# Kernel optimization log

Measured on AMD Instinct MI355X. Metric: run time of the kernel, lower is better.

## Reference

```python
import jax, jax.numpy as jnp
import numpy as np

TEMPERATURE = 0.1
BATCH_SIZE = 64
EPS = 1e-8  # torch.nn.CosineSimilarity eps
NEG_INF = -1e30

B, C, D = 64, 16, 512  # batch, children per sample, feature dim


def setup_inputs() -> dict:
    key = jax.random.key(0)
    k1, k2, k3, k4 = jax.random.split(key, 4)
    children_is = jax.random.normal(k1, (B, C, D), dtype=jnp.float32)
    children_js = jax.random.normal(k2, (B, C, D), dtype=jnp.float32)
    partnet_ids = jnp.arange(B, dtype=jnp.int64 if jax.config.jax_enable_x64 else jnp.int32)
    neg_idx_j = jax.random.randint(k3, (B, B, C), 0, C)  # negatives drawn from children_js
    neg_idx_k = jax.random.randint(k4, (B, B, C), 0, C)  # negatives drawn from children_is
    return {
        "children_is": children_is,
        "children_js": children_js,
        "partnet_ids": partnet_ids,
        "neg_idx_j": neg_idx_j,
        "neg_idx_k": neg_idx_k,
    }


def _safe_norm(x, axis=-1):
    return jnp.maximum(jnp.sqrt(jnp.sum(x * x, axis=axis)), EPS)


def _ntxent(ci, cj, pids, nj, nk):
    b = ci.shape[0]
    fi = ci.reshape(b, -1)  # [B, L] flattened anchors
    fj = cj.reshape(b, -1)  # [B, L] flattened positives
    norm_i = _safe_norm(fi)

    # positive: cos(flat(children_i), flat(children_j[i])) / T
    pos = jnp.sum(fi * fj, axis=-1) / (norm_i * _safe_norm(fj))  # [B]

    src = jnp.arange(b)[None, :, None]  # broadcast source-sample index
    # gathered negatives: g*[i, j] = children_*[j, neg_idx[i, j]] flattened -> [B, B, L]
    gj = cj[src, nj].reshape(b, b, -1)
    gk = ci[src, nk].reshape(b, b, -1)

    sim_j = jnp.einsum('il,ijl->ij', fi, gj) / (norm_i[:, None] * _safe_norm(gj))
    sim_k = jnp.einsum('il,ijl->ij', fi, gk) / (norm_i[:, None] * _safe_norm(gk))

    # negative pair valid iff j != i and partnet ids differ
    eye = jnp.arange(b)
    mask = (eye[None, :] != eye[:, None]) & (pids[None, :] != pids[:, None])  # [B, B]

    logits = jnp.concatenate(
        [pos[:, None],
         jnp.where(mask, sim_j, NEG_INF),
         jnp.where(mask, sim_k, NEG_INF)], axis=1) / TEMPERATURE  # [B, 1+2B]

    # CrossEntropy with label 0, reduction='sum' over the batch of anchors
    loss = jnp.sum(-logits[:, 0] + jax.scipy.special.logsumexp(logits, axis=1))
    return loss / (2.0 * BATCH_SIZE)


def reference(children_is, children_js, partnet_ids, neg_idx_j, neg_idx_k):
    return _ntxent(children_is, children_js, partnet_ids, neg_idx_j, neg_idx_k)
```

## Files before the change

### kernel.cpp

```cpp
#include <hip/hip_runtime.h>
#include <math.h>

#define BB 64
#define CC 16
#define DD 512
#define LL 8192
#define EPSV 1e-8f
#define INVT 10.0f
#define NEGINF_T (-1e31f)

#define WS_N2I 0
#define WS_N2J 1024
#define WS_DJ  2048
#define WS_DK  6144
#define WS_POS 10240

__device__ __forceinline__ float dot4(float4 a, float4 b) {
    return a.x * b.x + a.y * b.y + a.z * b.z + a.w * b.w;
}

__device__ __forceinline__ float wave_reduce(float v) {
    #pragma unroll
    for (int off = 32; off; off >>= 1) v += __shfl_down(v, off);
    return v;
}

__global__ __launch_bounds__(256) void ntx_prep(const float* __restrict__ ci,
                                                const float* __restrict__ cj,
                                                float* __restrict__ ws,
                                                float* __restrict__ out) {
    const int b = blockIdx.x, tid = threadIdx.x;
    __shared__ float red[4];
    if (b < 512) {
        const int row  = b * 4 + (tid >> 6);
        const int lane = tid & 63;
        const int r    = row & 1023;
        const float4* src = (const float4*)(row < 1024 ? ci : cj);
        float4 v1 = src[r * 128 + lane];
        float4 v2 = src[r * 128 + 64 + lane];
        float acc = dot4(v1, v1) + dot4(v2, v2);
        acc = wave_reduce(acc);
        if (lane == 0) ws[(row < 1024 ? WS_N2I : WS_N2J) + r] = acc;
    } else {
        const int i = b - 512;
        if (b == 512 && tid == 0) out[0] = 0.f;
        const float4* fi = (const float4*)(ci + i * LL);
        const float4* fj = (const float4*)(cj + i * LL);
        float acc = 0.f;
        #pragma unroll
        for (int it = 0; it < 8; ++it) acc += dot4(fi[tid + 256 * it], fj[tid + 256 * it]);
        acc = wave_reduce(acc);
        if ((tid & 63) == 0) red[tid >> 6] = acc;
        __syncthreads();
        if (tid == 0) ws[WS_POS + i] = red[0] + red[1] + red[2] + red[3];
    }
}

__global__ __launch_bounds__(256) void ntx_sim(const float* __restrict__ ci,
                                               const float* __restrict__ cj,
                                               const int* __restrict__ nj,
                                               const int* __restrict__ nk,
                                               float* __restrict__ ws) {
    const int jt  = blockIdx.x;
    const int i   = blockIdx.y;
    const int tid = threadIdx.x;

    __shared__ int   sidx[2][4][16];
    __shared__ float red[4][2][4];

    if (tid < 64)        ((int*)sidx)[tid] = nj[i * 1024 + jt * 64 + tid];
    else if (tid < 128)  ((int*)sidx)[tid] = nk[i * 1024 + jt * 64 + (tid - 64)];

    const float4* fi4 = (const float4*)(ci + i * LL);
    float4 fiv[8];
    #pragma unroll
    for (int it = 0; it < 8; ++it) fiv[it] = fi4[tid + 256 * it];

    __syncthreads();

    const int d4   = tid & 127;
    const int half = tid >> 7;
    const float4* cj4 = (const float4*)cj;
    const float4* ci4 = (const float4*)ci;

    #pragma unroll
    for (int jj = 0; jj < 4; ++jj) {
        const int j = jt * 4 + jj;
        const float4* bj = cj4 + j * CC * 128;
        const float4* bk = ci4 + j * CC * 128;
        float aj = 0.f, ak = 0.f;
        #pragma unroll
        for (int it = 0; it < 8; ++it) {
            const int c = half + 2 * it;
            float4 vj = bj[sidx[0][jj][c] * 128 + d4];
            float4 vk = bk[sidx[1][jj][c] * 128 + d4];
            aj += dot4(fiv[it], vj);
            ak += dot4(fiv[it], vk);
        }
        aj = wave_reduce(aj);
        ak = wave_reduce(ak);
        if ((tid & 63) == 0) { red[jj][0][tid >> 6] = aj; red[jj][1][tid >> 6] = ak; }
    }
    __syncthreads();
    if (tid < 8) {
        const int jj = tid >> 1, side = tid & 1;
        float s = red[jj][side][0] + red[jj][side][1] + red[jj][side][2] + red[jj][side][3];
        ws[(side ? WS_DK : WS_DJ) + i * BB + jt * 4 + jj] = s;
    }
}

__global__ __launch_bounds__(64) void ntx_final(const int* __restrict__ pids,
                                                const int* __restrict__ nj,
                                                const int* __restrict__ nk,
                                                const float* __restrict__ ws,
                                                float* __restrict__ out) {
    const int i = blockIdx.x, j = threadIdx.x;
    __shared__ float sn2i[1024], sn2j[1024];
    const float4* n2i4 = (const float4*)(ws + WS_N2I);
    const float4* n2j4 = (const float4*)(ws + WS_N2J);
    #pragma unroll
    for (int t = 0; t < 4; ++t) {
        ((float4*)sn2i)[j + 64 * t] = n2i4[j + 64 * t];
        ((float4*)sn2j)[j + 64 * t] = n2j4[j + 64 * t];
    }
    __syncthreads();

    float si = 0.f, sjf = 0.f;
    #pragma unroll
    for (int c = 0; c < CC; ++c) { si += sn2i[i * CC + c]; sjf += sn2j[i * CC + c]; }
    const float ni = fmaxf(sqrtf(si), EPSV);
    const float l0 = ws[WS_POS + i] / (ni * fmaxf(sqrtf(sjf), EPSV)) * INVT;

    float gj = 0.f, gk = 0.f;
    #pragma unroll
    for (int c = 0; c < CC; ++c) {
        gj += sn2j[j * CC + nj[(i * BB + j) * CC + c]];
        gk += sn2i[j * CC + nk[(i * BB + j) * CC + c]];
    }

    const bool valid = (j != i) && (pids[j] != pids[i]);
    float lj = NEGINF_T, lk = NEGINF_T;
    if (valid) {
        const float inv = INVT / ni;
        lj = ws[WS_DJ + i * BB + j] / fmaxf(sqrtf(gj), EPSV) * inv;
        lk = ws[WS_DK + i * BB + j] / fmaxf(sqrtf(gk), EPSV) * inv;
    }

    float m = fmaxf(lj, lk);
    #pragma unroll
    for (int off = 32; off; off >>= 1) m = fmaxf(m, __shfl_xor(m, off));
    m = fmaxf(m, l0);

    float s = __expf(lj - m) + __expf(lk - m);
    s = wave_reduce(s);
    if (j == 0) {
        s += __expf(l0 - m);
        const float loss_i = -l0 + m + __logf(s);
        atomicAdd(out, loss_i * (1.0f / (2.0f * BB)));
    }
}

extern "C" void kernel_launch(void* const* d_in, const int* in_sizes, int n_in,
                              void* d_out, int out_size, void* d_ws, size_t ws_size,
                              hipStream_t stream) {
    const float* ci  = (const float*)d_in[0];
    const float* cj  = (const float*)d_in[1];
    const int*  pids = (const int*) d_in[2];
    const int*  nj   = (const int*) d_in[3];
    const int*  nk   = (const int*) d_in[4];
    float* ws  = (float*)d_ws;
    float* out = (float*)d_out;

    ntx_prep<<<576, 256, 0, stream>>>(ci, cj, ws, out);
    ntx_sim<<<dim3(16, BB), 256, 0, stream>>>(ci, cj, nj, nk, ws);
    ntx_final<<<BB, 64, 0, stream>>>(pids, nj, nk, ws, out);
}
```

Before: 79.84 us.

## Stage source sample in LDS and fuse norm/positive prep into sim kernel

```diff
diff --git a/kernel.cpp b/kernel.cpp
--- a/kernel.cpp
+++ b/kernel.cpp
@@ -25,87 +25,86 @@
     return v;
 }
 
-__global__ __launch_bounds__(256) void ntx_prep(const float* __restrict__ ci,
-                                                const float* __restrict__ cj,
-                                                float* __restrict__ ws,
-                                                float* __restrict__ out) {
-    const int b = blockIdx.x, tid = threadIdx.x;
-    __shared__ float red[4];
-    if (b < 512) {
-        const int row  = b * 4 + (tid >> 6);
-        const int lane = tid & 63;
-        const int r    = row & 1023;
-        const float4* src = (const float4*)(row < 1024 ? ci : cj);
-        float4 v1 = src[r * 128 + lane];
-        float4 v2 = src[r * 128 + 64 + lane];
-        float acc = dot4(v1, v1) + dot4(v2, v2);
-        acc = wave_reduce(acc);
-        if (lane == 0) ws[(row < 1024 ? WS_N2I : WS_N2J) + r] = acc;
-    } else {
-        const int i = b - 512;
-        if (b == 512 && tid == 0) out[0] = 0.f;
-        const float4* fi = (const float4*)(ci + i * LL);
-        const float4* fj = (const float4*)(cj + i * LL);
-        float acc = 0.f;
-        #pragma unroll
-        for (int it = 0; it < 8; ++it) acc += dot4(fi[tid + 256 * it], fj[tid + 256 * it]);
-        acc = wave_reduce(acc);
-        if ((tid & 63) == 0) red[tid >> 6] = acc;
-        __syncthreads();
-        if (tid == 0) ws[WS_POS + i] = red[0] + red[1] + red[2] + red[3];
-    }
-}
-
 __global__ __launch_bounds__(256) void ntx_sim(const float* __restrict__ ci,
                                                const float* __restrict__ cj,
                                                const int* __restrict__ nj,
                                                const int* __restrict__ nk,
-                                               float* __restrict__ ws) {
-    const int jt  = blockIdx.x;
-    const int i   = blockIdx.y;
+                                               float* __restrict__ ws,
+                                               float* __restrict__ out) {
+    const int j   = blockIdx.x;
+    const int ig  = blockIdx.y;
     const int tid = threadIdx.x;
 
-    __shared__ int   sidx[2][4][16];
-    __shared__ float red[4][2][4];
+    __shared__ float scj[LL];
+    __shared__ float sci[LL];
+    __shared__ int   sidx[2][8][CC];
 
-    if (tid < 64)        ((int*)sidx)[tid] = nj[i * 1024 + jt * 64 + tid];
-    else if (tid < 128)  ((int*)sidx)[tid] = nk[i * 1024 + jt * 64 + (tid - 64)];
-
-    const float4* fi4 = (const float4*)(ci + i * LL);
-    float4 fiv[8];
+    float4* s4j = (float4*)scj;
+    float4* s4i = (float4*)sci;
+    const float4* gcj = (const float4*)(cj + j * LL);
+    const float4* gci = (const float4*)(ci + j * LL);
     #pragma unroll
-    for (int it = 0; it < 8; ++it) fiv[it] = fi4[tid + 256 * it];
-
+    for (int t = 0; t < 8; ++t) {
+        s4j[tid + 256 * t] = gcj[tid + 256 * t];
+        s4i[tid + 256 * t] = gci[tid + 256 * t];
+    }
+    {
+        const int t = tid >> 5, side = (tid >> 4) & 1, c = tid & 15;
+        const int i = ig + 8 * t;
+        const int* src = side ? nk : nj;
+        sidx[side][t][c] = src[(i * BB + j) * CC + c];
+    }
+    if (j == 0 && ig == 0 && tid == 0) out[0] = 0.f;
     __syncthreads();
 
-    const int d4   = tid & 127;
-    const int half = tid >> 7;
-    const float4* cj4 = (const float4*)cj;
-    const float4* ci4 = (const float4*)ci;
+    const int wave = tid >> 6, lane = tid & 63;
+
+    if (ig == 0) {
+        #pragma unroll
+        for (int r8 = 0; r8 < 8; ++r8) {
+            const int r  = wave * 8 + r8;
+            const int rr = r & 15;
+            const float4* src = (r < 16) ? s4j : s4i;
+            float4 a = src[rr * 128 + lane];
+            float4 b = src[rr * 128 + 64 + lane];
+            float acc = dot4(a, a) + dot4(b, b);
+            acc = wave_reduce(acc);
+            if (lane == 0) ws[(r < 16 ? WS_N2J : WS_N2I) + j * CC + rr] = acc;
+        }
+    }
 
     #pragma unroll
-    for (int jj = 0; jj < 4; ++jj) {
-        const int j = jt * 4 + jj;
-        const float4* bj = cj4 + j * CC * 128;
-        const float4* bk = ci4 + j * CC * 128;
-        float aj = 0.f, ak = 0.f;
+    for (int tt = 0; tt < 2; ++tt) {
+        const int t = 2 * wave + tt;
+        const int i = ig + 8 * t;
+        const float4* fi4 = (const float4*)(ci + i * LL);
+        const bool diag = (i == j);
+        float aj = 0.f, ak = 0.f, ap = 0.f;
         #pragma unroll
-        for (int it = 0; it < 8; ++it) {
-            const int c = half + 2 * it;
-            float4 vj = bj[sidx[0][jj][c] * 128 + d4];
-            float4 vk = bk[sidx[1][jj][c] * 128 + d4];
-            aj += dot4(fiv[it], vj);
-            ak += dot4(fiv[it], vk);
+        for (int c = 0; c < CC; ++c) {
+            const int rj = sidx[0][t][c];
+            const int rk = sidx[1][t][c];
+            #pragma unroll
+            for (int h = 0; h < 2; ++h) {
+                const int o = h * 64 + lane;
+                float4 fv = fi4[c * 128 + o];
+                float4 vj = s4j[rj * 128 + o];
+                float4 vk = s4i[rk * 128 + o];
+                aj += dot4(fv, vj);
+                ak += dot4(fv, vk);
+                if (diag) ap += dot4(fv, s4j[c * 128 + o]);
+            }
         }
         aj = wave_reduce(aj);
         ak = wave_reduce(ak);
-        if ((tid & 63) == 0) { red[jj][0][tid >> 6] = aj; red[jj][1][tid >> 6] = ak; }
-    }
-    __syncthreads();
-    if (tid < 8) {
-        const int jj = tid >> 1, side = tid & 1;
-        float s = red[jj][side][0] + red[jj][side][1] + red[jj][side][2] + red[jj][side][3];
-        ws[(side ? WS_DK : WS_DJ) + i * BB + jt * 4 + jj] = s;
+        if (lane == 0) {
+            ws[WS_DJ + i * BB + j] = aj;
+            ws[WS_DK + i * BB + j] = ak;
+        }
+        if (diag) {
+            ap = wave_reduce(ap);
+            if (lane == 0) ws[WS_POS + i] = ap;
+        }
     }
 }
 
@@ -171,7 +170,6 @@
     float* ws  = (float*)d_ws;
     float* out = (float*)d_out;
 
-    ntx_prep<<<576, 256, 0, stream>>>(ci, cj, ws, out);
-    ntx_sim<<<dim3(16, BB), 256, 0, stream>>>(ci, cj, nj, nk, ws);
+    ntx_sim<<<dim3(BB, 8), 256, 0, stream>>>(ci, cj, nj, nk, ws, out);
     ntx_final<<<BB, 64, 0, stream>>>(pids, nj, nk, ws, out);
 }
```

New measurement: 82.62 us. 1.03x slower.

## Replace gathered dot products with bf16 MFMA all-pairs row GEMM

Applied to the files above, without the earlier changes.

```diff
diff --git a/kernel.cpp b/kernel.cpp
--- a/kernel.cpp
+++ b/kernel.cpp
@@ -9,38 +9,51 @@
 #define INVT 10.0f
 #define NEGINF_T (-1e31f)
 
-#define WS_N2I 0
-#define WS_N2J 1024
-#define WS_DJ  2048
-#define WS_DK  6144
-#define WS_POS 10240
+#define OFF_CIB 0
+#define OFF_CJB (1u << 20)
+#define OFF_D   (2u << 20)
+#define OFF_N2I (10u << 20)
+#define OFF_N2J ((10u << 20) + 4096u)
+#define OFF_POS ((10u << 20) + 8192u)
+
+typedef short bf16x8 __attribute__((ext_vector_type(8)));
+typedef float f32x4  __attribute__((ext_vector_type(4)));
 
 __device__ __forceinline__ float dot4(float4 a, float4 b) {
     return a.x * b.x + a.y * b.y + a.z * b.z + a.w * b.w;
 }
-
 __device__ __forceinline__ float wave_reduce(float v) {
     #pragma unroll
     for (int off = 32; off; off >>= 1) v += __shfl_down(v, off);
     return v;
 }
+__device__ __forceinline__ unsigned short f2bf(float f) {
+    union { float f; unsigned u; } x; x.f = f;
+    return (unsigned short)((x.u + 0x7fffu + ((x.u >> 16) & 1u)) >> 16);
+}
 
 __global__ __launch_bounds__(256) void ntx_prep(const float* __restrict__ ci,
                                                 const float* __restrict__ cj,
-                                                float* __restrict__ ws,
+                                                char* __restrict__ ws,
                                                 float* __restrict__ out) {
     const int b = blockIdx.x, tid = threadIdx.x;
+    const int wave = tid >> 6, lane = tid & 63;
     __shared__ float red[4];
+
     if (b < 512) {
-        const int row  = b * 4 + (tid >> 6);
-        const int lane = tid & 63;
-        const int r    = row & 1023;
-        const float4* src = (const float4*)(row < 1024 ? ci : cj);
-        float4 v1 = src[r * 128 + lane];
-        float4 v2 = src[r * 128 + 64 + lane];
-        float acc = dot4(v1, v1) + dot4(v2, v2);
-        acc = wave_reduce(acc);
-        if (lane == 0) ws[(row < 1024 ? WS_N2I : WS_N2J) + r] = acc;
+        const int r  = b * 4 + wave;
+        const int rr = r & 1023;
+        const bool is_i = (r < 1024);
+        const float* src = is_i ? ci : cj;
+        unsigned short* dst = (unsigned short*)(ws + (is_i ? OFF_CIB : OFF_CJB));
+        float4 v1 = ((const float4*)(src + rr * DD))[lane];
+        float4 v2 = ((const float4*)(src + rr * DD))[64 + lane];
+        float acc = wave_reduce(dot4(v1, v1) + dot4(v2, v2));
+        if (lane == 0) ((float*)(ws + (is_i ? OFF_N2I : OFF_N2J)))[rr] = acc;
+        ushort4 h1 = { f2bf(v1.x), f2bf(v1.y), f2bf(v1.z), f2bf(v1.w) };
+        ushort4 h2 = { f2bf(v2.x), f2bf(v2.y), f2bf(v2.z), f2bf(v2.w) };
+        ((ushort4*)(dst + rr * DD))[lane]      = h1;
+        ((ushort4*)(dst + rr * DD))[64 + lane] = h2;
     } else {
         const int i = b - 512;
         if (b == 512 && tid == 0) out[0] = 0.f;
@@ -50,100 +63,101 @@
         #pragma unroll
         for (int it = 0; it < 8; ++it) acc += dot4(fi[tid + 256 * it], fj[tid + 256 * it]);
         acc = wave_reduce(acc);
-        if ((tid & 63) == 0) red[tid >> 6] = acc;
+        if (lane == 0) red[wave] = acc;
         __syncthreads();
-        if (tid == 0) ws[WS_POS + i] = red[0] + red[1] + red[2] + red[3];
+        if (tid == 0) ((float*)(ws + OFF_POS))[i] = red[0] + red[1] + red[2] + red[3];
     }
 }
 
-__global__ __launch_bounds__(256) void ntx_sim(const float* __restrict__ ci,
-                                               const float* __restrict__ cj,
-                                               const int* __restrict__ nj,
-                                               const int* __restrict__ nk,
-                                               float* __restrict__ ws) {
-    const int jt  = blockIdx.x;
-    const int i   = blockIdx.y;
+__global__ __launch_bounds__(256) void ntx_gemm(const char* __restrict__ ws_c,
+                                                float* __restrict__ D) {
+    const int bm = blockIdx.x;
+    const int bn = blockIdx.y;
     const int tid = threadIdx.x;
+    const int wave = tid >> 6, lane = tid & 63;
+    const int wm = wave >> 1, wn = wave & 1;
+    const int quad = lane >> 4, lr = lane & 15;
 
-    __shared__ int   sidx[2][4][16];
-    __shared__ float red[4][2][4];
+    const short* A = (const short*)(ws_c + OFF_CIB);
+    const bool isj = (bn < 16);
+    const short* B = (const short*)(ws_c + (isj ? OFF_CJB : OFF_CIB));
+    const int row0 = bm * 64 + wm * 32;
+    const int nrow0 = (isj ? bn : bn - 16) * 64 + wn * 32;
 
-    if (tid < 64)        ((int*)sidx)[tid] = nj[i * 1024 + jt * 64 + tid];
-    else if (tid < 128)  ((int*)sidx)[tid] = nk[i * 1024 + jt * 64 + (tid - 64)];
+    f32x4 acc[2][2] = {};
+    const int ka = quad * 8;
 
-    const float4* fi4 = (const float4*)(ci + i * LL);
-    float4 fiv[8];
+    #pragma unroll 4
+    for (int kk = 0; kk < 16; ++kk) {
+        const int k = kk * 32 + ka;
+        bf16x8 a0 = *(const bf16x8*)(A + (row0 + lr) * DD + k);
+        bf16x8 a1 = *(const bf16x8*)(A + (row0 + 16 + lr) * DD + k);
+        bf16x8 b0 = *(const bf16x8*)(B + (nrow0 + lr) * DD + k);
+        bf16x8 b1 = *(const bf16x8*)(B + (nrow0 + 16 + lr) * DD + k);
+        acc[0][0] = __builtin_amdgcn_mfma_f32_16x16x32_bf16(a0, b0, acc[0][0], 0, 0, 0);
+        acc[0][1] = __builtin_amdgcn_mfma_f32_16x16x32_bf16(a0, b1, acc[0][1], 0, 0, 0);
+        acc[1][0] = __builtin_amdgcn_mfma_f32_16x16x32_bf16(a1, b0, acc[1][0], 0, 0, 0);
+        acc[1][1] = __builtin_amdgcn_mfma_f32_16x16x32_bf16(a1, b1, acc[1][1], 0, 0, 0);
+    }
+
+    const int gcol0 = bn * 64 + wn * 32;
     #pragma unroll
-    for (int it = 0; it < 8; ++it) fiv[it] = fi4[tid + 256 * it];
-
-    __syncthreads();
-
-    const int d4   = tid & 127;
-    const int half = tid >> 7;
-    const float4* cj4 = (const float4*)cj;
-    const float4* ci4 = (const float4*)ci;
-
-    #pragma unroll
-    for (int jj = 0; jj < 4; ++jj) {
-        const int j = jt * 4 + jj;
-        const float4* bj = cj4 + j * CC * 128;
-        const float4* bk = ci4 + j * CC * 128;
-        float aj = 0.f, ak = 0.f;
+    for (int a = 0; a < 2; ++a) {
         #pragma unroll
-        for (int it = 0; it < 8; ++it) {
-            const int c = half + 2 * it;
-            float4 vj = bj[sidx[0][jj][c] * 128 + d4];
-            float4 vk = bk[sidx[1][jj][c] * 128 + d4];
-            aj += dot4(fiv[it], vj);
-            ak += dot4(fiv[it], vk);
+        for (int b = 0; b < 2; ++b) {
+            const int row = row0 + a * 16 + quad * 4;
+            const int col = gcol0 + b * 16 + lr;
+            #pragma unroll
+            for (int r = 0; r < 4; ++r)
+                D[(row + r) * 2048 + col] = acc[a][b][r];
         }
-        aj = wave_reduce(aj);
-        ak = wave_reduce(ak);
-        if ((tid & 63) == 0) { red[jj][0][tid >> 6] = aj; red[jj][1][tid >> 6] = ak; }
-    }
-    __syncthreads();
-    if (tid < 8) {
-        const int jj = tid >> 1, side = tid & 1;
-        float s = red[jj][side][0] + red[jj][side][1] + red[jj][side][2] + red[jj][side][3];
-        ws[(side ? WS_DK : WS_DJ) + i * BB + jt * 4 + jj] = s;
     }
 }
 
 __global__ __launch_bounds__(64) void ntx_final(const int* __restrict__ pids,
                                                 const int* __restrict__ nj,
                                                 const int* __restrict__ nk,
-                                                const float* __restrict__ ws,
+                                                const char* __restrict__ ws_c,
                                                 float* __restrict__ out) {
     const int i = blockIdx.x, j = threadIdx.x;
-    __shared__ float sn2i[1024], sn2j[1024];
-    const float4* n2i4 = (const float4*)(ws + WS_N2I);
-    const float4* n2j4 = (const float4*)(ws + WS_N2J);
-    #pragma unroll
-    for (int t = 0; t < 4; ++t) {
-        ((float4*)sn2i)[j + 64 * t] = n2i4[j + 64 * t];
-        ((float4*)sn2j)[j + 64 * t] = n2j4[j + 64 * t];
-    }
-    __syncthreads();
+    const float* D   = (const float*)(ws_c + OFF_D);
+    const float* n2i = (const float*)(ws_c + OFF_N2I);
+    const float* n2j = (const float*)(ws_c + OFF_N2J);
+    const float* pos = (const float*)(ws_c + OFF_POS);
 
     float si = 0.f, sjf = 0.f;
     #pragma unroll
-    for (int c = 0; c < CC; ++c) { si += sn2i[i * CC + c]; sjf += sn2j[i * CC + c]; }
+    for (int c = 0; c < CC; ++c) { si += n2i[i * CC + c]; sjf += n2j[i * CC + c]; }
     const float ni = fmaxf(sqrtf(si), EPSV);
-    const float l0 = ws[WS_POS + i] / (ni * fmaxf(sqrtf(sjf), EPSV)) * INVT;
+    const float l0 = pos[i] / (ni * fmaxf(sqrtf(sjf), EPSV)) * INVT;
 
-    float gj = 0.f, gk = 0.f;
+    int4 njv[4], nkv[4];
     #pragma unroll
-    for (int c = 0; c < CC; ++c) {
-        gj += sn2j[j * CC + nj[(i * BB + j) * CC + c]];
-        gk += sn2i[j * CC + nk[(i * BB + j) * CC + c]];
+    for (int t = 0; t < 4; ++t) {
+        njv[t] = ((const int4*)(nj + (i * BB + j) * CC))[t];
+        nkv[t] = ((const int4*)(nk + (i * BB + j) * CC))[t];
+    }
+    float gj = 0.f, gk = 0.f, dj = 0.f, dk = 0.f;
+    #pragma unroll
+    for (int t = 0; t < 4; ++t) {
+        const int aj[4] = { njv[t].x, njv[t].y, njv[t].z, njv[t].w };
+        const int ak[4] = { nkv[t].x, nkv[t].y, nkv[t].z, nkv[t].w };
+        #pragma unroll
+        for (int u = 0; u < 4; ++u) {
+            const int c = t * 4 + u;
+            gj += n2j[j * CC + aj[u]];
+            gk += n2i[j * CC + ak[u]];
+            dj += D[(i * CC + c) * 2048 + j * CC + aj[u]];
+            dk += D[(i * CC + c) * 2048 + 1024 + j * CC + ak[u]];
+        }
     }
 
     const bool valid = (j != i) && (pids[j] != pids[i]);
     float lj = NEGINF_T, lk = NEGINF_T;
     if (valid) {
         const float inv = INVT / ni;
-        lj = ws[WS_DJ + i * BB + j] / fmaxf(sqrtf(gj), EPSV) * inv;
-        lk = ws[WS_DK + i * BB + j] / fmaxf(sqrtf(gk), EPSV) * inv;
+        lj = dj / fmaxf(sqrtf(gj), EPSV) * inv;
+        lk = dk / fmaxf(sqrtf(gk), EPSV) * inv;
     }
 
     float m = fmaxf(lj, lk);
@@ -168,10 +182,10 @@
     const int*  pids = (const int*) d_in[2];
     const int*  nj   = (const int*) d_in[3];
     const int*  nk   = (const int*) d_in[4];
-    float* ws  = (float*)d_ws;
+    char*  ws  = (char*)d_ws;
     float* out = (float*)d_out;
 
     ntx_prep<<<576, 256, 0, stream>>>(ci, cj, ws, out);
-    ntx_sim<<<dim3(16, BB), 256, 0, stream>>>(ci, cj, nj, nk, ws);
+    ntx_gemm<<<dim3(16, 32), 256, 0, stream>>>(ws, (float*)(ws + OFF_D));
     ntx_final<<<BB, 64, 0, stream>>>(pids, nj, nk, ws, out);
 }
```

Result: slower. 88.33 us (+10.6%).
